# Optimization experiments

Measured on AMD Instinct MI355X. Metric: run time of the kernel, lower is better.

## Reference

```python
import jax, jax.numpy as jnp
import numpy as np

B, T, F = 256, 2048, 20
H_NODES = 256


def _heaviside(x):
    # smooth heaviside approx used throughout the original module
    return (jnp.tanh(10.0 * x) + 1.0) * 0.5


def _evap(wu, wl, wd, pet):
    h = _heaviside
    et1 = h(wu - pet) * pet + h(pet - wu) * wu
    rp = h(pet - et1) * (pet - et1)  # h(-(pet-et1))*0 term vanishes
    et22 = h(rp - wl) * wl + h(wl - rp) * rp
    et2 = h(rp) * et22
    et33 = h(rp - et2 - wd) * wd + h(wd - (rp - et2)) * (rp - et2)
    et3 = h(rp - et2) * et33
    return et1, et2, et3


def _runoff(wu, wl, wd, p, wum, wlm, wdm, b, c):
    wum = wum * 19.9 + 0.1
    wlm = wlm * 30.0 + 60.0
    wdm = wdm * 60.0 + 60.0
    c = c * 0.19 + 0.01
    b = b * 0.3 + 0.1
    w_total = wum + wlm + wdm
    s = c * (wu / w_total) ** 2 + b * (wl / w_total) ** 2
    return _heaviside(p - s) * (p - s)


def _partition(runoff, k1, k2, k3):
    k1 = k1 * 0.69 + 0.01
    k2 = k2 * 0.69 + 0.01
    k3 = k3 * 0.89 + 0.01
    sr = k1 * runoff
    itf = k2 * (runoff - sr)
    bf = k3 * (runoff - sr - itf)
    return sr, itf, bf


def setup_inputs() -> dict:
    key = jax.random.key(0)
    ks = jax.random.split(key, 7)
    u = lambda k, shp: jax.random.uniform(k, shp, jnp.float32, -0.05, 0.05)
    inputs = jax.random.uniform(ks[0], (B, T, F), jnp.float32)
    return {
        "inputs": inputs,
        "w1": u(ks[1], (15, H_NODES)),
        "b1": jnp.zeros((H_NODES,), jnp.float32),
        "w2": u(ks[2], (H_NODES, 64)),
        "b2": jnp.zeros((64,), jnp.float32),
        "w3": u(ks[3], (64, 8)),
        "b3": jnp.zeros((8,), jnp.float32),
    }


def reference(inputs, w1, b1, w2, b2, w3, b3):
    pet = inputs[..., 0:1]
    tmean = inputs[..., 1:2]
    p = inputs[..., 2:3]
    attrs = inputs[..., 5:]  # [B,T,15]

    # static-attribute -> physical-parameter MLP
    h1 = jnp.tanh(attrs @ w1 + b1)
    h2 = jnp.tanh(h1 @ w2 + b2)
    params = jax.nn.sigmoid(h2 @ w3 + b3)  # [B,T,8]

    xs = jnp.concatenate([pet, p, tmean, params], axis=-1)  # [B,T,11]

    def step(state, x):
        wu, wl, wd = state[:, 0:1], state[:, 1:2], state[:, 2:3]
        pet_t, p_t = x[:, 0:1], x[:, 1:2]
        et1, et2, et3 = _evap(wu, wl, wd, pet_t)
        clip = lambda d: jnp.clip(d, -1e5, 1e5)
        wu_n = wu + clip(p_t - et1)
        wl_n = wl + clip(p_t - et1 - et2)
        wd_n = wd + clip(p_t - et1 - et2 - et3)
        ns = jnp.concatenate([wu_n, wl_n, wd_n], axis=1)  # [B,3]
        return ns, ns

    init = jnp.zeros((inputs.shape[0], 3), inputs.dtype)
    _, outs = jax.lax.scan(step, init, jnp.swapaxes(xs, 0, 1))  # [T,B,3]
    outputs = jnp.swapaxes(outs, 0, 1)  # [B,T,3]

    wu, wl, wd = outputs[..., 0:1], outputs[..., 1:2], outputs[..., 2:3]
    wum, wlm, wdm = params[..., 0:1], params[..., 1:2], params[..., 2:3]
    b, c = params[..., 3:4], params[..., 4:5]
    k1, k2, k3 = params[..., 5:6], params[..., 6:7], params[..., 7:8]

    et1, et2, et3 = _evap(wu, wl, wd, pet)
    # NOTE: original call() swaps (wl,wd) and (wlm,wdm) here - kept faithful
    runoff = _runoff(wu, wd, wl, p, wum, wdm, wlm, b, c)
    sr, itf, bf = _partition(runoff, k1, k2, k3)
    total_q = sr + itf * 0.5 + bf * 0.25  # flow routing
    return total_q  # [B,T,1]
```

## Files before the change

### kernel.cpp

```cpp
#include <hip/hip_runtime.h>

#define B_ 256
#define T_ 2048
#define F_ 20
#define NT (B_*T_)
#define CH 16
#define NCH (T_/CH)

typedef __bf16 bf16x8 __attribute__((ext_vector_type(8)));
typedef float  f32x4  __attribute__((ext_vector_type(4)));

__device__ __forceinline__ float ex2(float x){ return __builtin_amdgcn_exp2f(x); }
__device__ __forceinline__ float rcpf_(float x){ return __builtin_amdgcn_rcpf(x); }

#define K10F 28.853900817779268f
#define K1F   2.8853900817779268f
#define LOG2E 1.4426950408889634f

__device__ __forceinline__ float hside(float x){ return 1.0f - rcpf_(ex2(K10F*x) + 1.0f); }
__device__ __forceinline__ float tanh_f(float z){ return 1.0f - 2.0f*rcpf_(ex2(K1F*z) + 1.0f); }
__device__ __forceinline__ float sigmoid_f(float z){ return rcpf_(1.0f + ex2(-LOG2E*z)); }


__global__ __launch_bounds__(256) void prep_kernel(const float* __restrict__ in,
                                                   float* __restrict__ ws){
  int r = blockIdx.x*256 + threadIdx.x;
  if (r >= NT) return;
  int b = r & (B_-1);
  int t = r >> 8;
  const float* src = in + ((size_t)b*T_ + t)*F_;
  ((float2*)ws)[r] = make_float2(src[0], src[2]);
}

__global__ __launch_bounds__(512) void fused_kernel(const float* __restrict__ in,
    const float* __restrict__ w1, const float* __restrict__ b1,
    const float* __restrict__ w2, const float* __restrict__ b2,
    const float* __restrict__ w3, const float* __restrict__ b3,
    float* __restrict__ ws){
  extern __shared__ char sm[];
  float* pk4 = ws + 4*(size_t)NT;

  if (blockIdx.x < 4) {
    asm volatile("s_setprio 3");
    const float2* pp2 = (const float2*)ws;
    float* wuT = ws + 2*(size_t)NT;
    float* wdT = ws + 3*(size_t)NT;
    float*  d1L = (float*)sm;
    float*  bsQ = (float*)(sm + 8192);
    float2* rhL = (float2*)(sm + 24576);
    float2* qbL = (float2*)(sm + 40960);

    int tid = threadIdx.x;
    int wv = tid >> 6, lane = tid & 63;
    int boff = blockIdx.x * 64;

    float wu = 0.0f, wl = 0.0f, wd = 0.0f;
    float2 buf[2][8];

    if (wv == 0){
      #pragma unroll
      for (int g = 0; g < 2; ++g)
        #pragma unroll
        for (int i = 0; i < 8; ++i)
          buf[g][i] = pp2[(g*8 + i)*B_ + boff + lane];
    }

    for (int it = 0; it < NCH + 3; ++it){
      if (wv == 0){
        if (it < NCH){
          int c = it, par = c & 1;
          #pragma unroll
          for (int g = 0; g < 2; ++g){
            #pragma unroll
            for (int i = 0; i < 8; ++i){
              int s = g*8 + i;
              float pet = buf[g][i].x, p = buf[g][i].y;
              float d  = wu - pet;
              float r1 = rcpf_(ex2(K10F*d) + 1.0f);
              float d1 = -d*r1;
              float base = (p - pet) + d1;
              wu += base;
              wuT[(c*CH + s)*B_ + boff + lane] = wu;
              d1L[par*(CH*64) + s*64 + lane] = d1;
              bsQ[(c&3)*(CH*64) + s*64 + lane] = base;
            }
            int cn = (c + 1 < NCH) ? c + 1 : c;
            #pragma unroll
            for (int i = 0; i < 8; ++i)
              buf[g][i] = pp2[(cn*CH + g*8 + i)*B_ + boff + lane];
          }
        }
      } else if (wv == 1){
        if (it >= 1 && it <= NCH){
          int c = it - 1, par = c & 1;
          #pragma unroll
          for (int s = 0; s < CH; ++s){
            float d1 = d1L[par*(CH*64) + s*64 + lane];
            float r2 = rcpf_(ex2(K10F*d1) + 1.0f);
            float rp = fmaf(-d1, r2, d1);
            float hrp = 1.0f - rcpf_(ex2(K10F*rp) + 1.0f);
            rhL[par*(CH*64) + s*64 + lane] = make_float2(rp, hrp);
          }
        }
      } else if (wv == 2){
        if (it >= 2 && it <= NCH + 1){
          int c = it - 2, par = c & 1;
          #pragma unroll
          for (int s = 0; s < CH; ++s){
            float2 rh  = rhL[par*(CH*64) + s*64 + lane];
            float base = bsQ[(c&3)*(CH*64) + s*64 + lane];
            float d2   = rh.x - wl;
            float r    = rcpf_(ex2(K10F*d2) + 1.0f);
            float et22 = fmaf(d2, r, wl);
            float et2  = rh.y * et22;
            float b2v  = base - et2;
            wl += b2v;
            qbL[par*(CH*64) + s*64 + lane] = make_float2(rh.x - et2, b2v);
          }
        }
      } else if (wv == 3){
        if (it >= 3){
          int c = it - 3, par = c & 1;
          #pragma unroll
          for (int s = 0; s < CH; ++s){
            float2 qb  = qbL[par*(CH*64) + s*64 + lane];
            float hqv  = 1.0f - rcpf_(ex2(K10F*qb.x) + 1.0f);
            float d3   = qb.x - wd;
            float r    = rcpf_(ex2(K10F*d3) + 1.0f);
            float et33 = fmaf(d3, r, wd);
            float et3  = hqv * et33;
            wd += qb.y - et3;
            wdT[(c*CH + s)*B_ + boff + lane] = wd;
          }
        }
      }
      __syncthreads();
    }
    return;
  }

  __bf16* w1f   = (__bf16*)sm;
  __bf16* w2f   = (__bf16*)(sm + 8192);
  float*  b1s   = (float*)(sm + 24576);
  float*  b2s   = (float*)(sm + 25600);
  float*  b3s   = (float*)(sm + 25856);
  __bf16* hbufA = (__bf16*)(sm + 25888);

  int tid  = threadIdx.x;
  int lane = tid & 63;
  int wv   = tid >> 6;
  int m    = lane & 15;
  int q    = lane >> 4;
  int r0   = (blockIdx.x - 4)*256 + wv*32;

  bf16x8 a1[2];
  #pragma unroll
  for (int u = 0; u < 2; ++u){
    int rowA = r0 + u*16 + m;
    int bA = rowA & (B_-1), tA = rowA >> 8;
    const float* ap = in + ((size_t)bA*T_ + tA)*F_ + 5;
    #pragma unroll
    for (int j = 0; j < 8; ++j){
      int k = q*8 + j;
      a1[u][j] = (__bf16)((k < 15) ? ap[k] : 0.0f);
    }
  }
  bf16x8 w3h[2], w3l[2];
  #pragma unroll
  for (int kb = 0; kb < 2; ++kb){
    #pragma unroll
    for (int j = 0; j < 8; ++j){
      float v = (m < 8) ? w3[(kb*32 + q*8 + j)*8 + m] : 0.0f;
      __bf16 hi = (__bf16)v;
      w3h[kb][j] = hi;
      w3l[kb][j] = (__bf16)(v - (float)hi);
    }
  }

  ((float4*)sm)[tid] = make_float4(0.0f, 0.0f, 0.0f, 0.0f);
  __syncthreads();
  for (int idx = tid; idx < 15*256; idx += 512){
    int k = idx >> 8, n = idx & 255;
    int ct = n >> 4;
    int l  = ((k>>3)*16) + (n & 15);
    int j  = k & 7;
    w1f[(ct*32 + l)*8 + j] = (__bf16)w1[idx];
  }
  for (int idx = tid; idx < 8192; idx += 512){
    int kk = idx >> 6, n = idx & 63;
    int kb2 = kk >> 5;
    int lq  = (kk >> 3) & 3;
    int j   = kk & 7;
    int ct  = n >> 4;
    int l   = lq*16 + (n & 15);
    w2f[((kb2*4 + ct)*64 + l)*8 + j] = (__bf16)w2[kk*64 + n];
  }
  if (tid < 256) b1s[tid] = b1[tid];
  if (tid < 64)  b2s[tid] = b2[tid];
  if (tid < 8)   b3s[tid] = b3[tid];
  __syncthreads();

  f32x4 zero4 = {0.0f, 0.0f, 0.0f, 0.0f};
  bf16x8 zero8;
  #pragma unroll
  for (int j = 0; j < 8; ++j) zero8[j] = (__bf16)0.0f;

  __bf16* hb = hbufA + wv*2304;
  f32x4 acc2[2][4] = {{zero4, zero4, zero4, zero4},
                      {zero4, zero4, zero4, zero4}};

  #pragma unroll
  for (int pc = 0; pc < 2; ++pc){
    if (pc == 1){
      __syncthreads();
      for (int idx = tid; idx < 8192; idx += 512){
        int kk = idx >> 6, n = idx & 63;
        int kb2 = kk >> 5;
        int lq  = (kk >> 3) & 3;
        int j   = kk & 7;
        int ct  = n >> 4;
        int l   = lq*16 + (n & 15);
        w2f[((kb2*4 + ct)*64 + l)*8 + j] = (__bf16)w2[(128 + kk)*64 + n];
      }
      __syncthreads();
    }
    #pragma unroll
    for (int ph = 0; ph < 2; ++ph){
      int p = pc*2 + ph;
      #pragma unroll
      for (int c4 = 0; c4 < 4; ++c4){
        int ct = p*4 + c4;
        bf16x8 bw = zero8;
        if (lane < 32) bw = *(const bf16x8*)&w1f[(ct*32 + lane)*8];
        int f = c4*16 + m;
        float bb = b1s[p*64 + f];
        #pragma unroll
        for (int u = 0; u < 2; ++u){
          f32x4 c1 = __builtin_amdgcn_mfma_f32_16x16x32_bf16(a1[u], bw, zero4, 0, 0, 0);
          #pragma unroll
          for (int i = 0; i < 4; ++i){
            float h = tanh_f(c1[i] + bb);
            hb[(u*16 + q*4 + i)*72 + f] = (__bf16)h;
          }
        }
      }
      #pragma unroll
      for (int kb = 0; kb < 2; ++kb){
        bf16x8 a2_0 = *(const bf16x8*)&hb[ m      *72 + kb*32 + q*8];
        bf16x8 a2_1 = *(const bf16x8*)&hb[(16 + m)*72 + kb*32 + q*8];
        #pragma unroll
        for (int ct = 0; ct < 4; ++ct){
          bf16x8 bw2 = *(const bf16x8*)&w2f[(((ph*2 + kb)*4 + ct)*64 + lane)*8];
          acc2[0][ct] = __builtin_amdgcn_mfma_f32_16x16x32_bf16(a2_0, bw2, acc2[0][ct], 0, 0, 0);
          acc2[1][ct] = __builtin_amdgcn_mfma_f32_16x16x32_bf16(a2_1, bw2, acc2[1][ct], 0, 0, 0);
        }
      }
    }
  }

  #pragma unroll
  for (int ct = 0; ct < 4; ++ct){
    int f = ct*16 + m;
    float bb = b2s[f];
    #pragma unroll
    for (int u = 0; u < 2; ++u)
      #pragma unroll
      for (int i = 0; i < 4; ++i){
        float h = tanh_f(acc2[u][ct][i] + bb);
        hb[(u*16 + q*4 + i)*72 + f] = (__bf16)h;
      }
  }

  f32x4 acc3[2] = {zero4, zero4};
  #pragma unroll
  for (int kb = 0; kb < 2; ++kb){
    bf16x8 a3_0 = *(const bf16x8*)&hb[ m      *72 + kb*32 + q*8];
    bf16x8 a3_1 = *(const bf16x8*)&hb[(16 + m)*72 + kb*32 + q*8];
    acc3[0] = __builtin_amdgcn_mfma_f32_16x16x32_bf16(a3_0, w3h[kb], acc3[0], 0, 0, 0);
    acc3[0] = __builtin_amdgcn_mfma_f32_16x16x32_bf16(a3_0, w3l[kb], acc3[0], 0, 0, 0);
    acc3[1] = __builtin_amdgcn_mfma_f32_16x16x32_bf16(a3_1, w3h[kb], acc3[1], 0, 0, 0);
    acc3[1] = __builtin_amdgcn_mfma_f32_16x16x32_bf16(a3_1, w3l[kb], acc3[1], 0, 0, 0);
  }

  float* hf = (float*)hb;
  if (m < 8){
    float bb3 = b3s[m];
    #pragma unroll
    for (int u = 0; u < 2; ++u)
      #pragma unroll
      for (int i = 0; i < 4; ++i)
        hf[(u*16 + q*4 + i)*9 + m] = sigmoid_f(acc3[u][i] + bb3);
  }
  if (lane < 32){
    const float* Pr = hf + lane*9;
    float P0=Pr[0], P1=Pr[1], P2=Pr[2], P3=Pr[3];
    float P4=Pr[4], P5=Pr[5], P6=Pr[6], P7=Pr[7];
    float wum = fmaf(P0, 19.9f, 0.1f);
    float wlm = fmaf(P2, 30.0f, 60.0f);
    float wdm = fmaf(P1, 60.0f, 60.0f);
    float wt  = wum + wlm + wdm;
    float rw  = 1.0f / wt;
    float cc  = fmaf(P4, 0.19f, 0.01f);
    float bc  = fmaf(P3, 0.30f, 0.10f);
    float A   = cc*rw*rw;
    float Bc  = bc*rw*rw;
    float k1  = fmaf(P5, 0.69f, 0.01f);
    float k2  = fmaf(P6, 0.69f, 0.01f);
    float k3  = fmaf(P7, 0.89f, 0.01f);
    float KP  = k1 + 0.5f*k2*(1.0f-k1) + 0.25f*k3*(1.0f-k1)*(1.0f-k2);
    *(float4*)&pk4[(size_t)(r0 + lane)*4] = make_float4(A, Bc, KP, 0.0f);
  }
}

__global__ __launch_bounds__(256) void final_kernel(const float* __restrict__ ws,
                                                    float* __restrict__ out){
  __shared__ float tile[64*65];
  int tb = blockIdx.x & 31;
  int bb = blockIdx.x >> 5;
  int t0 = tb*64, b0 = bb*64;
  int tid = threadIdx.x;
  const float2* pp2 = (const float2*)ws;
  const float* wuT  = ws + 2*(size_t)NT;
  const float* wdT  = ws + 3*(size_t)NT;
  const float* pk4  = ws + 4*(size_t)NT;

  #pragma unroll
  for (int k = 0; k < 16; ++k){
    int idx = k*256 + tid;
    int tl = idx >> 6, bl = idx & 63;
    int r = (t0 + tl)*B_ + b0 + bl;
    float p  = pp2[r].y;
    float wu = wuT[r], wd = wdT[r];
    float4 k4 = *(const float4*)&pk4[(size_t)r*4];
    float ps = p - k4.x*wu*wu - k4.y*wd*wd;
    float runoff = hside(ps)*ps;
    tile[bl*65 + tl] = k4.z * runoff;
  }
  __syncthreads();
  #pragma unroll
  for (int k = 0; k < 16; ++k){
    int idx = k*256 + tid;
    int tl2 = idx & 63, bl2 = idx >> 6;
    out[(size_t)(b0 + bl2)*T_ + t0 + tl2] = tile[bl2*65 + tl2];
  }
}

extern "C" void kernel_launch(void* const* d_in, const int* in_sizes, int n_in,
                              void* d_out, int out_size, void* d_ws, size_t ws_size,
                              hipStream_t stream) {
  const float* in = (const float*)d_in[0];
  const float* w1 = (const float*)d_in[1];
  const float* b1 = (const float*)d_in[2];
  const float* w2 = (const float*)d_in[3];
  const float* b2 = (const float*)d_in[4];
  const float* w3 = (const float*)d_in[5];
  const float* b3 = (const float*)d_in[6];
  float* out = (float*)d_out;
  float* ws  = (float*)d_ws;

  prep_kernel <<<NT/256,     256, 0,     stream>>>(in, ws);
  fused_kernel<<<NT/256 + 4, 512, 62752, stream>>>(in, w1, b1, w2, b2, w3, b3, ws);
  final_kernel<<<128,        256, 0,     stream>>>(ws, out);
}
```

Baseline: 215.6 us.

## Rebalance scan pipeline into three wave stages with 32-step chunks

Reorganizes the sequential bucket-state scan from a four-wave pipeline into three waves. The rp computation moves into the wu wave, and the hrp and wl update are merged into one stage. The chunk size doubles to 32 steps, which halves the number of block-wide barriers and cuts the pipeline fill from three stages to two. The cost is a longer per-step critical path in the first and second waves, plus raising dynamic shared memory to 64 KB for all blocks, which may reduce occupancy of the MLP blocks.

```diff
diff --git a/kernel.cpp b/kernel.cpp
--- a/kernel.cpp
+++ b/kernel.cpp
@@ -4,8 +4,6 @@
 #define T_ 2048
 #define F_ 20
 #define NT (B_*T_)
-#define CH 16
-#define NCH (T_/CH)
 
 typedef __bf16 bf16x8 __attribute__((ext_vector_type(8)));
 typedef float  f32x4  __attribute__((ext_vector_type(4)));
@@ -45,10 +43,8 @@
     const float2* pp2 = (const float2*)ws;
     float* wuT = ws + 2*(size_t)NT;
     float* wdT = ws + 3*(size_t)NT;
-    float*  d1L = (float*)sm;
-    float*  bsQ = (float*)(sm + 8192);
-    float2* rhL = (float2*)(sm + 24576);
-    float2* qbL = (float2*)(sm + 40960);
+    float2* abL = (float2*)sm;
+    float2* qbL = (float2*)(sm + 32768);
 
     int tid = threadIdx.x;
     int wv = tid >> 6, lane = tid & 63;
@@ -59,78 +55,77 @@
 
     if (wv == 0){
       #pragma unroll
-      for (int g = 0; g < 2; ++g)
-        #pragma unroll
-        for (int i = 0; i < 8; ++i)
-          buf[g][i] = pp2[(g*8 + i)*B_ + boff + lane];
-    }
-
-    for (int it = 0; it < NCH + 3; ++it){
+      for (int i = 0; i < 8; ++i){
+        buf[0][i] = pp2[(    i)*B_ + boff + lane];
+        buf[1][i] = pp2[(8 + i)*B_ + boff + lane];
+      }
+    }
+
+    for (int it = 0; it < 66; ++it){
       if (wv == 0){
-        if (it < NCH){
+        if (it < 64){
           int c = it, par = c & 1;
           #pragma unroll
-          for (int g = 0; g < 2; ++g){
+          for (int g = 0; g < 4; ++g){
             #pragma unroll
             for (int i = 0; i < 8; ++i){
               int s = g*8 + i;
-              float pet = buf[g][i].x, p = buf[g][i].y;
+              float pet = buf[g&1][i].x, p = buf[g&1][i].y;
               float d  = wu - pet;
               float r1 = rcpf_(ex2(K10F*d) + 1.0f);
               float d1 = -d*r1;
               float base = (p - pet) + d1;
               wu += base;
-              wuT[(c*CH + s)*B_ + boff + lane] = wu;
-              d1L[par*(CH*64) + s*64 + lane] = d1;
-              bsQ[(c&3)*(CH*64) + s*64 + lane] = base;
+              wuT[(c*32 + s)*B_ + boff + lane] = wu;
+              float r2 = rcpf_(ex2(K10F*d1) + 1.0f);
+              float rp = fmaf(-d1, r2, d1);
+              abL[(par*32 + s)*64 + lane] = make_float2(rp, base);
             }
-            int cn = (c + 1 < NCH) ? c + 1 : c;
+            int gn = c*4 + g + 2;
+            if (gn > 255) gn = 255;
             #pragma unroll
             for (int i = 0; i < 8; ++i)
-              buf[g][i] = pp2[(cn*CH + g*8 + i)*B_ + boff + lane];
+              buf[g&1][i] = pp2[(gn*8 + i)*B_ + boff + lane];
           }
         }
       } else if (wv == 1){
-        if (it >= 1 && it <= NCH){
+        if (it >= 1 && it <= 64){
           int c = it - 1, par = c & 1;
-          #pragma unroll
-          for (int s = 0; s < CH; ++s){
-            float d1 = d1L[par*(CH*64) + s*64 + lane];
-            float r2 = rcpf_(ex2(K10F*d1) + 1.0f);
-            float rp = fmaf(-d1, r2, d1);
-            float hrp = 1.0f - rcpf_(ex2(K10F*rp) + 1.0f);
-            rhL[par*(CH*64) + s*64 + lane] = make_float2(rp, hrp);
+          #pragma unroll 1
+          for (int half = 0; half < 2; ++half){
+            #pragma unroll
+            for (int s0 = 0; s0 < 16; ++s0){
+              int s = half*16 + s0;
+              float2 ab  = abL[(par*32 + s)*64 + lane];
+              float rp   = ab.x, base = ab.y;
+              float hrp  = 1.0f - rcpf_(ex2(K10F*rp) + 1.0f);
+              float d2   = rp - wl;
+              float r    = rcpf_(ex2(K10F*d2) + 1.0f);
+              float et22 = fmaf(d2, r, wl);
+              float et2  = hrp * et22;
+              float b2v  = base - et2;
+              wl += b2v;
+              qbL[(par*32 + s)*64 + lane] = make_float2(rp - et2, b2v);
+            }
           }
         }
       } else if (wv == 2){
-        if (it >= 2 && it <= NCH + 1){
+        if (it >= 2){
           int c = it - 2, par = c & 1;
-          #pragma unroll
-          for (int s = 0; s < CH; ++s){
-            float2 rh  = rhL[par*(CH*64) + s*64 + lane];
-            float base = bsQ[(c&3)*(CH*64) + s*64 + lane];
-            float d2   = rh.x - wl;
-            float r    = rcpf_(ex2(K10F*d2) + 1.0f);
-            float et22 = fmaf(d2, r, wl);
-            float et2  = rh.y * et22;
-            float b2v  = base - et2;
-            wl += b2v;
-            qbL[par*(CH*64) + s*64 + lane] = make_float2(rh.x - et2, b2v);
-          }
-        }
-      } else if (wv == 3){
-        if (it >= 3){
-          int c = it - 3, par = c & 1;
-          #pragma unroll
-          for (int s = 0; s < CH; ++s){
-            float2 qb  = qbL[par*(CH*64) + s*64 + lane];
-            float hqv  = 1.0f - rcpf_(ex2(K10F*qb.x) + 1.0f);
-            float d3   = qb.x - wd;
-            float r    = rcpf_(ex2(K10F*d3) + 1.0f);
-            float et33 = fmaf(d3, r, wd);
-            float et3  = hqv * et33;
-            wd += qb.y - et3;
-            wdT[(c*CH + s)*B_ + boff + lane] = wd;
+          #pragma unroll 1
+          for (int half = 0; half < 2; ++half){
+            #pragma unroll
+            for (int s0 = 0; s0 < 16; ++s0){
+              int s = half*16 + s0;
+              float2 qb  = qbL[(par*32 + s)*64 + lane];
+              float hqv  = 1.0f - rcpf_(ex2(K10F*qb.x) + 1.0f);
+              float d3   = qb.x - wd;
+              float r    = rcpf_(ex2(K10F*d3) + 1.0f);
+              float et33 = fmaf(d3, r, wd);
+              float et3  = hqv * et33;
+              wd += qb.y - et3;
+              wdT[(c*32 + s)*B_ + boff + lane] = wd;
+            }
           }
         }
       }
@@ -358,7 +353,14 @@
   float* out = (float*)d_out;
   float* ws  = (float*)d_ws;
 
+  static bool attr_set = false;
+  if (!attr_set){
+    hipFuncSetAttribute((const void*)fused_kernel,
+                        hipFuncAttributeMaxDynamicSharedMemorySize, 65536);
+    attr_set = true;
+  }
+
   prep_kernel <<<NT/256,     256, 0,     stream>>>(in, ws);
-  fused_kernel<<<NT/256 + 4, 512, 62752, stream>>>(in, w1, b1, w2, b2, w3, b3, ws);
+  fused_kernel<<<NT/256 + 4, 512, 65536, stream>>>(in, w1, b1, w2, b2, w3, b3, ws);
   final_kernel<<<128,        256, 0,     stream>>>(ws, out);
 }
```

Result: slower. 221.6 us (+2.8%).

## Merge MLP and final kernels into persistent cooperative kernel with grid sync

Applied to the files above, without the earlier changes.

Replaces the fused MLP kernel and the final output kernel with a single cooperative persistent kernel. Scan blocks and persistent MLP tile loops run first, then a grid-wide sync is followed by the runoff and transpose epilogue, split across all blocks in smaller 16x64 tiles. The aim is to remove a kernel launch and let the epilogue start as soon as the scan finishes. The cost is that each MLP tile now reloads and reformats w2 twice per tile with extra block barriers. The grid size is also capped, so far fewer blocks share the MLP work.

```diff
diff --git a/kernel.cpp b/kernel.cpp
--- a/kernel.cpp
+++ b/kernel.cpp
@@ -1,4 +1,7 @@
 #include <hip/hip_runtime.h>
+#include <hip/hip_cooperative_groups.h>
+
+namespace cg = cooperative_groups;
 
 #define B_ 256
 #define T_ 2048
@@ -32,15 +35,18 @@
   ((float2*)ws)[r] = make_float2(src[0], src[2]);
 }
 
-__global__ __launch_bounds__(512) void fused_kernel(const float* __restrict__ in,
+__global__ __launch_bounds__(512, 4) void coop_kernel(const float* __restrict__ in,
     const float* __restrict__ w1, const float* __restrict__ b1,
     const float* __restrict__ w2, const float* __restrict__ b2,
     const float* __restrict__ w3, const float* __restrict__ b3,
-    float* __restrict__ ws){
+    float* __restrict__ ws, float* __restrict__ out){
   extern __shared__ char sm[];
   float* pk4 = ws + 4*(size_t)NT;
-
-  if (blockIdx.x < 4) {
+  int bid = blockIdx.x;
+  int nb  = gridDim.x;
+  int tid = threadIdx.x;
+
+  if (bid < 4) {
     asm volatile("s_setprio 3");
     const float2* pp2 = (const float2*)ws;
     float* wuT = ws + 2*(size_t)NT;
@@ -50,9 +56,8 @@
     float2* rhL = (float2*)(sm + 24576);
     float2* qbL = (float2*)(sm + 40960);
 
-    int tid = threadIdx.x;
     int wv = tid >> 6, lane = tid & 63;
-    int boff = blockIdx.x * 64;
+    int boff = bid * 64;
 
     float wu = 0.0f, wl = 0.0f, wd = 0.0f;
     float2 buf[2][8];
@@ -136,212 +141,204 @@
       }
       __syncthreads();
     }
-    return;
+    asm volatile("s_setprio 0");
+  } else {
+    __bf16* w1f   = (__bf16*)sm;
+    __bf16* w2f   = (__bf16*)(sm + 8192);
+    float*  b1s   = (float*)(sm + 24576);
+    float*  b2s   = (float*)(sm + 25600);
+    float*  b3s   = (float*)(sm + 25856);
+    __bf16* hbufA = (__bf16*)(sm + 25888);
+
+    int lane = tid & 63;
+    int wv   = tid >> 6;
+    int m    = lane & 15;
+    int q    = lane >> 4;
+
+    bf16x8 w3h[2], w3l[2];
+    #pragma unroll
+    for (int kb = 0; kb < 2; ++kb){
+      #pragma unroll
+      for (int j = 0; j < 8; ++j){
+        float v = (m < 8) ? w3[(kb*32 + q*8 + j)*8 + m] : 0.0f;
+        __bf16 hi = (__bf16)v;
+        w3h[kb][j] = hi;
+        w3l[kb][j] = (__bf16)(v - (float)hi);
+      }
+    }
+
+    ((float4*)sm)[tid] = make_float4(0.0f, 0.0f, 0.0f, 0.0f);
+    __syncthreads();
+    for (int idx = tid; idx < 15*256; idx += 512){
+      int k = idx >> 8, n = idx & 255;
+      int ct = n >> 4;
+      int l  = ((k>>3)*16) + (n & 15);
+      int j  = k & 7;
+      w1f[(ct*32 + l)*8 + j] = (__bf16)w1[idx];
+    }
+    if (tid < 256) b1s[tid] = b1[tid];
+    if (tid < 64)  b2s[tid] = b2[tid];
+    if (tid < 8)   b3s[tid] = b3[tid];
+
+    f32x4 zero4 = {0.0f, 0.0f, 0.0f, 0.0f};
+    bf16x8 zero8;
+    #pragma unroll
+    for (int j = 0; j < 8; ++j) zero8[j] = (__bf16)0.0f;
+
+    __bf16* hb = hbufA + wv*2304;
+
+    for (int tile = bid - 4; tile < 2048; tile += nb - 4){
+      int r0 = tile*256 + wv*32;
+
+      bf16x8 a1[2];
+      #pragma unroll
+      for (int u = 0; u < 2; ++u){
+        int rowA = r0 + u*16 + m;
+        int bA = rowA & (B_-1), tA = rowA >> 8;
+        const float* ap = in + ((size_t)bA*T_ + tA)*F_ + 5;
+        #pragma unroll
+        for (int j = 0; j < 8; ++j){
+          int k = q*8 + j;
+          a1[u][j] = (__bf16)((k < 15) ? ap[k] : 0.0f);
+        }
+      }
+
+      f32x4 acc2[2][4] = {{zero4, zero4, zero4, zero4},
+                          {zero4, zero4, zero4, zero4}};
+
+      #pragma unroll
+      for (int pc = 0; pc < 2; ++pc){
+        __syncthreads();
+        for (int idx = tid; idx < 8192; idx += 512){
+          int kk = idx >> 6, n = idx & 63;
+          int kb2 = kk >> 5;
+          int lq  = (kk >> 3) & 3;
+          int j   = kk & 7;
+          int ct  = n >> 4;
+          int l   = lq*16 + (n & 15);
+          w2f[((kb2*4 + ct)*64 + l)*8 + j] = (__bf16)w2[(pc*128 + kk)*64 + n];
+        }
+        __syncthreads();
+        #pragma unroll
+        for (int ph = 0; ph < 2; ++ph){
+          int p = pc*2 + ph;
+          #pragma unroll
+          for (int c4 = 0; c4 < 4; ++c4){
+            int ct = p*4 + c4;
+            bf16x8 bw = zero8;
+            if (lane < 32) bw = *(const bf16x8*)&w1f[(ct*32 + lane)*8];
+            int f = c4*16 + m;
+            float bb = b1s[p*64 + f];
+            #pragma unroll
+            for (int u = 0; u < 2; ++u){
+              f32x4 c1 = __builtin_amdgcn_mfma_f32_16x16x32_bf16(a1[u], bw, zero4, 0, 0, 0);
+              #pragma unroll
+              for (int i = 0; i < 4; ++i){
+                float h = tanh_f(c1[i] + bb);
+                hb[(u*16 + q*4 + i)*72 + f] = (__bf16)h;
+              }
+            }
+          }
+          #pragma unroll
+          for (int kb = 0; kb < 2; ++kb){
+            bf16x8 a2_0 = *(const bf16x8*)&hb[ m      *72 + kb*32 + q*8];
+            bf16x8 a2_1 = *(const bf16x8*)&hb[(16 + m)*72 + kb*32 + q*8];
+            #pragma unroll
+            for (int ct = 0; ct < 4; ++ct){
+              bf16x8 bw2 = *(const bf16x8*)&w2f[(((ph*2 + kb)*4 + ct)*64 + lane)*8];
+              acc2[0][ct] = __builtin_amdgcn_mfma_f32_16x16x32_bf16(a2_0, bw2, acc2[0][ct], 0, 0, 0);
+              acc2[1][ct] = __builtin_amdgcn_mfma_f32_16x16x32_bf16(a2_1, bw2, acc2[1][ct], 0, 0, 0);
+            }
+          }
+        }
+      }
+
+      #pragma unroll
+      for (int ct = 0; ct < 4; ++ct){
+        int f = ct*16 + m;
+        float bb = b2s[f];
+        #pragma unroll
+        for (int u = 0; u < 2; ++u)
+          #pragma unroll
+          for (int i = 0; i < 4; ++i){
+            float h = tanh_f(acc2[u][ct][i] + bb);
+            hb[(u*16 + q*4 + i)*72 + f] = (__bf16)h;
+          }
+      }
+
+      f32x4 acc3[2] = {zero4, zero4};
+      #pragma unroll
+      for (int kb = 0; kb < 2; ++kb){
+        bf16x8 a3_0 = *(const bf16x8*)&hb[ m      *72 + kb*32 + q*8];
+        bf16x8 a3_1 = *(const bf16x8*)&hb[(16 + m)*72 + kb*32 + q*8];
+        acc3[0] = __builtin_amdgcn_mfma_f32_16x16x32_bf16(a3_0, w3h[kb], acc3[0], 0, 0, 0);
+        acc3[0] = __builtin_amdgcn_mfma_f32_16x16x32_bf16(a3_0, w3l[kb], acc3[0], 0, 0, 0);
+        acc3[1] = __builtin_amdgcn_mfma_f32_16x16x32_bf16(a3_1, w3h[kb], acc3[1], 0, 0, 0);
+        acc3[1] = __builtin_amdgcn_mfma_f32_16x16x32_bf16(a3_1, w3l[kb], acc3[1], 0, 0, 0);
+      }
+
+      float* hf = (float*)hb;
+      if (m < 8){
+        float bb3 = b3s[m];
+        #pragma unroll
+        for (int u = 0; u < 2; ++u)
+          #pragma unroll
+          for (int i = 0; i < 4; ++i)
+            hf[(u*16 + q*4 + i)*9 + m] = sigmoid_f(acc3[u][i] + bb3);
+      }
+      if (lane < 32){
+        const float* Pr = hf + lane*9;
+        float P0=Pr[0], P1=Pr[1], P2=Pr[2], P3=Pr[3];
+        float P4=Pr[4], P5=Pr[5], P6=Pr[6], P7=Pr[7];
+        float wum = fmaf(P0, 19.9f, 0.1f);
+        float wlm = fmaf(P2, 30.0f, 60.0f);
+        float wdm = fmaf(P1, 60.0f, 60.0f);
+        float wt  = wum + wlm + wdm;
+        float rw  = 1.0f / wt;
+        float cc  = fmaf(P4, 0.19f, 0.01f);
+        float bc  = fmaf(P3, 0.30f, 0.10f);
+        float A   = cc*rw*rw;
+        float Bc  = bc*rw*rw;
+        float k1  = fmaf(P5, 0.69f, 0.01f);
+        float k2  = fmaf(P6, 0.69f, 0.01f);
+        float k3  = fmaf(P7, 0.89f, 0.01f);
+        float KP  = k1 + 0.5f*k2*(1.0f-k1) + 0.25f*k3*(1.0f-k1)*(1.0f-k2);
+        *(float4*)&pk4[(size_t)(r0 + lane)*4] = make_float4(A, Bc, KP, 0.0f);
+      }
+    }
   }
 
-  __bf16* w1f   = (__bf16*)sm;
-  __bf16* w2f   = (__bf16*)(sm + 8192);
-  float*  b1s   = (float*)(sm + 24576);
-  float*  b2s   = (float*)(sm + 25600);
-  float*  b3s   = (float*)(sm + 25856);
-  __bf16* hbufA = (__bf16*)(sm + 25888);
-
-  int tid  = threadIdx.x;
-  int lane = tid & 63;
-  int wv   = tid >> 6;
-  int m    = lane & 15;
-  int q    = lane >> 4;
-  int r0   = (blockIdx.x - 4)*256 + wv*32;
-
-  bf16x8 a1[2];
-  #pragma unroll
-  for (int u = 0; u < 2; ++u){
-    int rowA = r0 + u*16 + m;
-    int bA = rowA & (B_-1), tA = rowA >> 8;
-    const float* ap = in + ((size_t)bA*T_ + tA)*F_ + 5;
-    #pragma unroll
-    for (int j = 0; j < 8; ++j){
-      int k = q*8 + j;
-      a1[u][j] = (__bf16)((k < 15) ? ap[k] : 0.0f);
-    }
-  }
-  bf16x8 w3h[2], w3l[2];
-  #pragma unroll
-  for (int kb = 0; kb < 2; ++kb){
-    #pragma unroll
-    for (int j = 0; j < 8; ++j){
-      float v = (m < 8) ? w3[(kb*32 + q*8 + j)*8 + m] : 0.0f;
-      __bf16 hi = (__bf16)v;
-      w3h[kb][j] = hi;
-      w3l[kb][j] = (__bf16)(v - (float)hi);
-    }
-  }
-
-  ((float4*)sm)[tid] = make_float4(0.0f, 0.0f, 0.0f, 0.0f);
-  __syncthreads();
-  for (int idx = tid; idx < 15*256; idx += 512){
-    int k = idx >> 8, n = idx & 255;
-    int ct = n >> 4;
-    int l  = ((k>>3)*16) + (n & 15);
-    int j  = k & 7;
-    w1f[(ct*32 + l)*8 + j] = (__bf16)w1[idx];
-  }
-  for (int idx = tid; idx < 8192; idx += 512){
-    int kk = idx >> 6, n = idx & 63;
-    int kb2 = kk >> 5;
-    int lq  = (kk >> 3) & 3;
-    int j   = kk & 7;
-    int ct  = n >> 4;
-    int l   = lq*16 + (n & 15);
-    w2f[((kb2*4 + ct)*64 + l)*8 + j] = (__bf16)w2[kk*64 + n];
-  }
-  if (tid < 256) b1s[tid] = b1[tid];
-  if (tid < 64)  b2s[tid] = b2[tid];
-  if (tid < 8)   b3s[tid] = b3[tid];
-  __syncthreads();
-
-  f32x4 zero4 = {0.0f, 0.0f, 0.0f, 0.0f};
-  bf16x8 zero8;
-  #pragma unroll
-  for (int j = 0; j < 8; ++j) zero8[j] = (__bf16)0.0f;
-
-  __bf16* hb = hbufA + wv*2304;
-  f32x4 acc2[2][4] = {{zero4, zero4, zero4, zero4},
-                      {zero4, zero4, zero4, zero4}};
-
-  #pragma unroll
-  for (int pc = 0; pc < 2; ++pc){
-    if (pc == 1){
+  cg::this_grid().sync();
+
+  {
+    float* tile_f = (float*)sm;
+    const float2* pp2v = (const float2*)ws;
+    const float* wuT  = ws + 2*(size_t)NT;
+    const float* wdT  = ws + 3*(size_t)NT;
+
+    for (int v = bid; v < 512; v += nb){
+      int t0 = (v >> 2) * 16;
+      int b0 = (v & 3) * 64;
       __syncthreads();
-      for (int idx = tid; idx < 8192; idx += 512){
-        int kk = idx >> 6, n = idx & 63;
-        int kb2 = kk >> 5;
-        int lq  = (kk >> 3) & 3;
-        int j   = kk & 7;
-        int ct  = n >> 4;
-        int l   = lq*16 + (n & 15);
-        w2f[((kb2*4 + ct)*64 + l)*8 + j] = (__bf16)w2[(128 + kk)*64 + n];
+      #pragma unroll
+      for (int k = 0; k < 2; ++k){
+        int idx = k*512 + tid;
+        int tl = idx >> 6, bl = idx & 63;
+        int r = (t0 + tl)*B_ + b0 + bl;
+        float p  = pp2v[r].y;
+        float wu = wuT[r], wd = wdT[r];
+        float4 k4 = *(const float4*)&pk4[(size_t)r*4];
+        float ps = p - k4.x*wu*wu - k4.y*wd*wd;
+        tile_f[bl*17 + tl] = k4.z * hside(ps) * ps;
       }
       __syncthreads();
-    }
-    #pragma unroll
-    for (int ph = 0; ph < 2; ++ph){
-      int p = pc*2 + ph;
-      #pragma unroll
-      for (int c4 = 0; c4 < 4; ++c4){
-        int ct = p*4 + c4;
-        bf16x8 bw = zero8;
-        if (lane < 32) bw = *(const bf16x8*)&w1f[(ct*32 + lane)*8];
-        int f = c4*16 + m;
-        float bb = b1s[p*64 + f];
-        #pragma unroll
-        for (int u = 0; u < 2; ++u){
-          f32x4 c1 = __builtin_amdgcn_mfma_f32_16x16x32_bf16(a1[u], bw, zero4, 0, 0, 0);
-          #pragma unroll
-          for (int i = 0; i < 4; ++i){
-            float h = tanh_f(c1[i] + bb);
-            hb[(u*16 + q*4 + i)*72 + f] = (__bf16)h;
-          }
-        }
-      }
-      #pragma unroll
-      for (int kb = 0; kb < 2; ++kb){
-        bf16x8 a2_0 = *(const bf16x8*)&hb[ m      *72 + kb*32 + q*8];
-        bf16x8 a2_1 = *(const bf16x8*)&hb[(16 + m)*72 + kb*32 + q*8];
-        #pragma unroll
-        for (int ct = 0; ct < 4; ++ct){
-          bf16x8 bw2 = *(const bf16x8*)&w2f[(((ph*2 + kb)*4 + ct)*64 + lane)*8];
-          acc2[0][ct] = __builtin_amdgcn_mfma_f32_16x16x32_bf16(a2_0, bw2, acc2[0][ct], 0, 0, 0);
-          acc2[1][ct] = __builtin_amdgcn_mfma_f32_16x16x32_bf16(a2_1, bw2, acc2[1][ct], 0, 0, 0);
-        }
-      }
-    }
-  }
-
-  #pragma unroll
-  for (int ct = 0; ct < 4; ++ct){
-    int f = ct*16 + m;
-    float bb = b2s[f];
-    #pragma unroll
-    for (int u = 0; u < 2; ++u)
-      #pragma unroll
-      for (int i = 0; i < 4; ++i){
-        float h = tanh_f(acc2[u][ct][i] + bb);
-        hb[(u*16 + q*4 + i)*72 + f] = (__bf16)h;
-      }
-  }
-
-  f32x4 acc3[2] = {zero4, zero4};
-  #pragma unroll
-  for (int kb = 0; kb < 2; ++kb){
-    bf16x8 a3_0 = *(const bf16x8*)&hb[ m      *72 + kb*32 + q*8];
-    bf16x8 a3_1 = *(const bf16x8*)&hb[(16 + m)*72 + kb*32 + q*8];
-    acc3[0] = __builtin_amdgcn_mfma_f32_16x16x32_bf16(a3_0, w3h[kb], acc3[0], 0, 0, 0);
-    acc3[0] = __builtin_amdgcn_mfma_f32_16x16x32_bf16(a3_0, w3l[kb], acc3[0], 0, 0, 0);
-    acc3[1] = __builtin_amdgcn_mfma_f32_16x16x32_bf16(a3_1, w3h[kb], acc3[1], 0, 0, 0);
-    acc3[1] = __builtin_amdgcn_mfma_f32_16x16x32_bf16(a3_1, w3l[kb], acc3[1], 0, 0, 0);
-  }
-
-  float* hf = (float*)hb;
-  if (m < 8){
-    float bb3 = b3s[m];
-    #pragma unroll
-    for (int u = 0; u < 2; ++u)
-      #pragma unroll
-      for (int i = 0; i < 4; ++i)
-        hf[(u*16 + q*4 + i)*9 + m] = sigmoid_f(acc3[u][i] + bb3);
-  }
-  if (lane < 32){
-    const float* Pr = hf + lane*9;
-    float P0=Pr[0], P1=Pr[1], P2=Pr[2], P3=Pr[3];
-    float P4=Pr[4], P5=Pr[5], P6=Pr[6], P7=Pr[7];
-    float wum = fmaf(P0, 19.9f, 0.1f);
-    float wlm = fmaf(P2, 30.0f, 60.0f);
-    float wdm = fmaf(P1, 60.0f, 60.0f);
-    float wt  = wum + wlm + wdm;
-    float rw  = 1.0f / wt;
-    float cc  = fmaf(P4, 0.19f, 0.01f);
-    float bc  = fmaf(P3, 0.30f, 0.10f);
-    float A   = cc*rw*rw;
-    float Bc  = bc*rw*rw;
-    float k1  = fmaf(P5, 0.69f, 0.01f);
-    float k2  = fmaf(P6, 0.69f, 0.01f);
-    float k3  = fmaf(P7, 0.89f, 0.01f);
-    float KP  = k1 + 0.5f*k2*(1.0f-k1) + 0.25f*k3*(1.0f-k1)*(1.0f-k2);
-    *(float4*)&pk4[(size_t)(r0 + lane)*4] = make_float4(A, Bc, KP, 0.0f);
-  }
-}
-
-__global__ __launch_bounds__(256) void final_kernel(const float* __restrict__ ws,
-                                                    float* __restrict__ out){
-  __shared__ float tile[64*65];
-  int tb = blockIdx.x & 31;
-  int bb = blockIdx.x >> 5;
-  int t0 = tb*64, b0 = bb*64;
-  int tid = threadIdx.x;
-  const float2* pp2 = (const float2*)ws;
-  const float* wuT  = ws + 2*(size_t)NT;
-  const float* wdT  = ws + 3*(size_t)NT;
-  const float* pk4  = ws + 4*(size_t)NT;
-
-  #pragma unroll
-  for (int k = 0; k < 16; ++k){
-    int idx = k*256 + tid;
-    int tl = idx >> 6, bl = idx & 63;
-    int r = (t0 + tl)*B_ + b0 + bl;
-    float p  = pp2[r].y;
-    float wu = wuT[r], wd = wdT[r];
-    float4 k4 = *(const float4*)&pk4[(size_t)r*4];
-    float ps = p - k4.x*wu*wu - k4.y*wd*wd;
-    float runoff = hside(ps)*ps;
-    tile[bl*65 + tl] = k4.z * runoff;
-  }
-  __syncthreads();
-  #pragma unroll
-  for (int k = 0; k < 16; ++k){
-    int idx = k*256 + tid;
-    int tl2 = idx & 63, bl2 = idx >> 6;
-    out[(size_t)(b0 + bl2)*T_ + t0 + tl2] = tile[bl2*65 + tl2];
+      #pragma unroll
+      for (int k = 0; k < 2; ++k){
+        int idx = k*512 + tid;
+        int tl2 = idx & 15, bl2 = idx >> 4;
+        out[(size_t)(b0 + bl2)*T_ + t0 + tl2] = tile_f[bl2*17 + tl2];
+      }
+    }
   }
 }
 
@@ -358,7 +355,21 @@
   float* out = (float*)d_out;
   float* ws  = (float*)d_ws;
 
-  prep_kernel <<<NT/256,     256, 0,     stream>>>(in, ws);
-  fused_kernel<<<NT/256 + 4, 512, 62752, stream>>>(in, w1, b1, w2, b2, w3, b3, ws);
-  final_kernel<<<128,        256, 0,     stream>>>(ws, out);
+  static int coop_grid = 0;
+  if (coop_grid == 0){
+    int occ = 0;
+    hipError_t e = hipOccupancyMaxActiveBlocksPerMultiprocessor(&occ, (const void*)coop_kernel,
+                                                                512, 62752);
+    int g = (e == hipSuccess && occ > 0) ? occ * 256 : 256;
+    if (g > 512) g = 512;
+    if (g < 8)   g = 8;
+    coop_grid = g;
+  }
+
+  prep_kernel<<<NT/256, 256, 0, stream>>>(in, ws);
+
+  void* args[] = {(void*)&in, (void*)&w1, (void*)&b1, (void*)&w2, (void*)&b2,
+                  (void*)&w3, (void*)&b3, (void*)&ws, (void*)&out};
+  hipLaunchCooperativeKernel((const void*)coop_kernel, dim3(coop_grid), dim3(512),
+                             args, 62752, stream);
 }
```

New measurement: 259.0 us. 20.1% more time.
